# Kernel optimization log

Measured on AMD Instinct MI355X. Metric: run time of the kernel, lower is better.

Reference implementation:

```python
import jax, jax.numpy as jnp
import numpy as np

NUM_EMBEDDINGS = 8192
EMBEDDING_DIM = 512
COMMITMENT_COST = 0.25
BATCH = 32768


def setup_inputs() -> dict:
    key = jax.random.key(0)
    k_in, k_cb = jax.random.split(key)
    inputs = jax.random.normal(k_in, (BATCH, EMBEDDING_DIM), dtype=jnp.float32)
    # xavier_uniform_ on [num_embeddings, embedding_dim]
    limit = float(np.sqrt(6.0 / (NUM_EMBEDDINGS + EMBEDDING_DIM)))
    codebook = jax.random.uniform(k_cb, (NUM_EMBEDDINGS, EMBEDDING_DIM),
                                  dtype=jnp.float32, minval=-limit, maxval=limit)
    return {"inputs": inputs, "codebook": codebook}


def reference(inputs, codebook):
    # distances[b, n] = ||x_b||^2 + ||e_n||^2 - 2 x_b . e_n  (cdist^2 via matmul)
    distances = (jnp.sum(inputs ** 2, axis=1, keepdims=True)
                 + jnp.sum(codebook ** 2, axis=1)
                 - 2.0 * jnp.matmul(inputs, codebook.T))
    encoding_indices = jnp.argmin(distances, axis=1)  # [B]

    # one-hot @ codebook is just a row gather
    quantized = codebook[encoding_indices]  # [B, D]

    e_latent_loss = jnp.mean((jax.lax.stop_gradient(quantized) - inputs) ** 2)
    q_latent_loss = jnp.mean((quantized - jax.lax.stop_gradient(inputs)) ** 2)
    loss = q_latent_loss + COMMITMENT_COST * e_latent_loss

    # straight-through estimator
    quantized_st = inputs + jax.lax.stop_gradient(quantized - inputs)

    # avg_probs = mean over batch of one-hot encodings -> normalized bincount
    counts = jnp.zeros((NUM_EMBEDDINGS,), dtype=jnp.float32).at[encoding_indices].add(1.0)
    avg_probs = counts / BATCH
    perplexity = jnp.exp(-jnp.sum(avg_probs * jnp.log(avg_probs + 1e-10)))

    return quantized_st, loss, perplexity
```

## Files before the change

### kernel.cpp

```cpp
#include <hip/hip_runtime.h>
#include <math.h>

#define BATCH 32768
#define D 512
#define NE 8192
#define NSPLIT 4
#define ESPAN (NE / NSPLIT)
#define NT 64
#define KC 128
#define NPHASE ((ESPAN / NT) * 4)
#define MARGIN 1.6e-2f

typedef float    f32x4 __attribute__((ext_vector_type(4)));
typedef _Float16 f16x8 __attribute__((ext_vector_type(8)));

__device__ __forceinline__ void g2l16(const void* g, void* l) {
    __builtin_amdgcn_global_load_lds((const __attribute__((address_space(1))) void*)g,
                                     (__attribute__((address_space(3))) void*)l, 16, 0, 0);
}
__device__ __forceinline__ unsigned short f2h(float f) {
    union { _Float16 h; unsigned short u; } c; c.h = (_Float16)f; return c.u;
}

__global__ void vq_norms_kernel(const float* __restrict__ cb, float* __restrict__ norms) {
    int row  = blockIdx.x * 4 + (threadIdx.x >> 6);
    int lane = threadIdx.x & 63;
    const float4* p = (const float4*)(cb + (size_t)row * D);
    float s = 0.f;
#pragma unroll
    for (int i = 0; i < 2; ++i) {
        float4 v = p[lane + 64 * i];
        s += v.x * v.x + v.y * v.y + v.z * v.z + v.w * v.w;
    }
    for (int off = 32; off; off >>= 1) s += __shfl_down(s, off);
    if (lane == 0) norms[row] = s;
}

__global__ void vq_cvt_swz(const float* __restrict__ cb, unsigned short* __restrict__ eq) {
    int i = blockIdx.x * 256 + threadIdx.x;
    int n = i >> 6, g = i & 63;
    int ch = g >> 4;
    int sl = (g & 15) ^ (n & 15);
    const float4* sp = (const float4*)(cb + (size_t)n * D + g * 8);
    float4 a = sp[0], b = sp[1];
    ushort4* dp = (ushort4*)(eq + (size_t)n * D + ch * KC + sl * 8);
    dp[0] = make_ushort4(f2h(a.x), f2h(a.y), f2h(a.z), f2h(a.w));
    dp[1] = make_ushort4(f2h(b.x), f2h(b.y), f2h(b.z), f2h(b.w));
}

__global__ __launch_bounds__(256, 2)
void vq_topk2(const float* __restrict__ x, const unsigned short* __restrict__ eq,
              const float* __restrict__ norms, float4* __restrict__ cands) {
    __shared__ char arena[40960];
    unsigned short* es0 = (unsigned short*)arena;
    unsigned short* es1 = (unsigned short*)(arena + 16384);
    float*          nlds = (float*)(arena + 32768);

    const int t = threadIdx.x;
    const int w = t >> 6, lane = t & 63, l15 = lane & 15, l4 = lane >> 4;
    const int b = blockIdx.x;
    const int xcd = b & 7;
    const int sp  = xcd >> 1;
    const int rb  = ((b >> 3) << 1) | (xcd & 1);
    const size_t row0 = (size_t)rb * 128;
    const int nbase = sp * ESPAN;

#define STAGE(DST, STEP) do {                                                           \
        const int snt_ = (STEP) >> 2, sch_ = (STEP) & 3;                                \
        _Pragma("unroll")                                                               \
        for (int i_ = 0; i_ < 4; ++i_) {                                                \
            int c_ = i_ * 256 + t;                                                      \
            int row_ = c_ >> 4, sl_ = c_ & 15;                                          \
            g2l16(eq + (size_t)(nbase + snt_ * NT + row_) * D + sch_ * KC + sl_ * 8,    \
                  (DST) + (size_t)(i_ * 256 + w * 64) * 8);                             \
        }                                                                               \
    } while (0)

    STAGE(es0, 0);
#pragma unroll
    for (int i = 0; i < 2; ++i) {
        int c = i * 256 + t;
        g2l16(norms + nbase + c * 4, (char*)nlds + (size_t)(i * 256 + w * 64) * 16);
    }

    f16x8 af[2][16];
#pragma unroll
    for (int mi = 0; mi < 2; ++mi) {
        const float4* xp = (const float4*)(x + (row0 + w * 32 + mi * 16 + l15) * D);
#pragma unroll
        for (int ks = 0; ks < 16; ++ks) {
            float4 p0 = xp[ks * 8 + l4 * 2];
            float4 p1 = xp[ks * 8 + l4 * 2 + 1];
            f16x8 v;
            v[0] = (_Float16)p0.x; v[1] = (_Float16)p0.y;
            v[2] = (_Float16)p0.z; v[3] = (_Float16)p0.w;
            v[4] = (_Float16)p1.x; v[5] = (_Float16)p1.y;
            v[6] = (_Float16)p1.z; v[7] = (_Float16)p1.w;
            af[mi][ks] = v;
        }
    }

    float v1[8], v2[8];
    int   i1[8], i2[8];
#pragma unroll
    for (int s = 0; s < 8; ++s) { v1[s] = v2[s] = 3.4e38f; i1[s] = i2[s] = 0x7fffffff; }

    unsigned short* cur = es0;
    unsigned short* nxt = es1;

    for (int nt_ = 0; nt_ < ESPAN / NT; ++nt_) {
        f32x4 acc[2][4];
#pragma unroll
        for (int mi = 0; mi < 2; ++mi)
#pragma unroll
            for (int ni = 0; ni < 4; ++ni) acc[mi][ni] = (f32x4){0.f, 0.f, 0.f, 0.f};

#pragma unroll
        for (int ch = 0; ch < 4; ++ch) {
            const int step = nt_ * 4 + ch;
            asm volatile("s_waitcnt vmcnt(0)" ::: "memory");
            __builtin_amdgcn_s_barrier();
            __builtin_amdgcn_sched_barrier(0);
            if (step + 1 < NPHASE) STAGE(nxt, step + 1);
            __builtin_amdgcn_s_setprio(1);
#pragma unroll
            for (int ksb = 0; ksb < 4; ++ksb) {
                f16x8 bfr[4];
#pragma unroll
                for (int ni = 0; ni < 4; ++ni) {
                    int slot = ((ksb << 2) | l4) ^ l15;
                    bfr[ni] = *(const f16x8*)((const char*)cur + ni * 4096 + l15 * 256 + slot * 16);
                }
#pragma unroll
                for (int mi = 0; mi < 2; ++mi)
#pragma unroll
                    for (int ni = 0; ni < 4; ++ni)
                        acc[mi][ni] = __builtin_amdgcn_mfma_f32_16x16x32_f16(
                            af[mi][ch * 4 + ksb], bfr[ni], acc[mi][ni], 0, 0, 0);
            }
            __builtin_amdgcn_s_setprio(0);
            unsigned short* tswap = cur; cur = nxt; nxt = tswap;
        }

        const int n0 = nbase + nt_ * NT;
        float nn[4];
#pragma unroll
        for (int ni = 0; ni < 4; ++ni) nn[ni] = nlds[nt_ * 64 + ni * 16 + l15];
#pragma unroll
        for (int mi = 0; mi < 2; ++mi)
#pragma unroll
            for (int r = 0; r < 4; ++r) {
                int s = mi * 4 + r;
#pragma unroll
                for (int ni = 0; ni < 4; ++ni) {
                    float dd = fmaf(-2.f, acc[mi][ni][r], nn[ni]);
                    int   cc = n0 + ni * 16 + l15;
                    if (dd < v2[s]) {
                        bool b1 = dd < v1[s];
                        v2[s] = b1 ? v1[s] : dd; i2[s] = b1 ? i1[s] : cc;
                        v1[s] = b1 ? dd : v1[s]; i1[s] = b1 ? cc : i1[s];
                    }
                }
            }
    }
#undef STAGE

#pragma unroll
    for (int s = 0; s < 8; ++s) {
        int mi = s >> 2, r = s & 3;
        size_t rowc = row0 + w * 32 + mi * 16 + l4 * 4 + r;
        cands[rowc * 64 + sp * 16 + l15] =
            make_float4(v1[s], __int_as_float(i1[s]), v2[s], __int_as_float(i2[s]));
    }
}

__global__ __launch_bounds__(512)
void vq_finish(const float* __restrict__ x, const float* __restrict__ cb,
               const float* __restrict__ norms, const float4* __restrict__ cands,
               float* __restrict__ counts, float* __restrict__ psum, float* __restrict__ out) {
    __shared__ float red[8];
    const int t = threadIdx.x, w = t >> 6, lane = t & 63;
    const size_t row = (size_t)blockIdx.x * 8 + w;

    float4 c4 = cands[row * 64 + lane];
    float va = c4.x, vb = c4.z;
    int   ia = __float_as_int(c4.y), ib = __float_as_int(c4.w);
    float m = fminf(va, vb);
#pragma unroll
    for (int off = 1; off < 64; off <<= 1) m = fminf(m, __shfl_xor(m, off));
    const float thr = m + MARGIN;

    const float4* xp = (const float4*)(x + row * D);
    float4 xa = xp[lane * 2], xb = xp[lane * 2 + 1];

    float bd = 3.4e38f; int bi = 0x7fffffff;
#pragma unroll 1
    for (int q = 0; q < 2; ++q) {
        unsigned long long mk = __ballot((q == 0 ? va : vb) <= thr);
        while (mk) {
            int src = __builtin_ctzll(mk);
            mk &= mk - 1;
            int ci = __shfl(q == 0 ? ia : ib, src);
            const float4* ep = (const float4*)(cb + (size_t)ci * D);
            float4 ea = ep[lane * 2], eb = ep[lane * 2 + 1];
            float s = 0.f;
            s = fmaf(xa.x, ea.x, s); s = fmaf(xa.y, ea.y, s);
            s = fmaf(xa.z, ea.z, s); s = fmaf(xa.w, ea.w, s);
            s = fmaf(xb.x, eb.x, s); s = fmaf(xb.y, eb.y, s);
            s = fmaf(xb.z, eb.z, s); s = fmaf(xb.w, eb.w, s);
#pragma unroll
            for (int off = 1; off < 64; off <<= 1) s += __shfl_xor(s, off);
            float dd = fmaf(-2.f, s, norms[ci]);
            if (dd < bd || (dd == bd && ci < bi)) { bd = dd; bi = ci; }
        }
    }

    const float4* qp = (const float4*)(cb + (size_t)bi * D);
    float4 qa = qp[lane * 2], qb = qp[lane * 2 + 1];
    float4* op = (float4*)(out + row * D);
    float s2 = 0.f;
    float4 oa, ob;
    {
        float d0 = qa.x - xa.x; oa.x = xa.x + d0; s2 = fmaf(d0, d0, s2);
        float d1 = qa.y - xa.y; oa.y = xa.y + d1; s2 = fmaf(d1, d1, s2);
        float d2 = qa.z - xa.z; oa.z = xa.z + d2; s2 = fmaf(d2, d2, s2);
        float d3 = qa.w - xa.w; oa.w = xa.w + d3; s2 = fmaf(d3, d3, s2);
        float d4 = qb.x - xb.x; ob.x = xb.x + d4; s2 = fmaf(d4, d4, s2);
        float d5 = qb.y - xb.y; ob.y = xb.y + d5; s2 = fmaf(d5, d5, s2);
        float d6 = qb.z - xb.z; ob.z = xb.z + d6; s2 = fmaf(d6, d6, s2);
        float d7 = qb.w - xb.w; ob.w = xb.w + d7; s2 = fmaf(d7, d7, s2);
    }
    op[lane * 2] = oa; op[lane * 2 + 1] = ob;
    for (int off = 32; off; off >>= 1) s2 += __shfl_down(s2, off);
    if (lane == 0) {
        red[w] = s2;
        atomicAdd(&counts[bi], 1.0f);
    }
    __syncthreads();
    if (t == 0) {
        float s = 0.f;
#pragma unroll
        for (int i = 0; i < 8; ++i) s += red[i];
        psum[blockIdx.x] = s;
    }
}

__global__ void vq_finalize_kernel(const float* __restrict__ counts, const float* __restrict__ psum,
                                   float* __restrict__ out2) {
    __shared__ float rede[256];
    __shared__ float reds[256];
    float se = 0.f, ss = 0.f;
    for (int i = threadIdx.x; i < NE; i += 256) {
        float p = counts[i] * (1.0f / (float)BATCH);
        se += p * logf(p + 1e-10f);
    }
    for (int i = threadIdx.x; i < 4096; i += 256) ss += psum[i];
    rede[threadIdx.x] = se; reds[threadIdx.x] = ss;
    __syncthreads();
    for (int off = 128; off; off >>= 1) {
        if (threadIdx.x < off) {
            rede[threadIdx.x] += rede[threadIdx.x + off];
            reds[threadIdx.x] += reds[threadIdx.x + off];
        }
        __syncthreads();
    }
    if (threadIdx.x == 0) {
        out2[0] = 1.25f * reds[0] * (1.0f / (float)((size_t)BATCH * D));
        out2[1] = expf(-rede[0]);
    }
}

#define BM 64
#define BN 64
#define BK 16
#define LDSP 68
__global__ __launch_bounds__(256)
void vq_argmin_kernel(const float* __restrict__ x, const float* __restrict__ cb,
                      const float* __restrict__ norms, int* __restrict__ out_idx) {
    __shared__ float xs[BK * LDSP];
    __shared__ float es[BK * LDSP];
    __shared__ float rv[BM][16];
    __shared__ int   ri[BM][16];
    const int t = threadIdx.x, tx = t & 15, ty = t >> 4;
    const int row0 = blockIdx.x * BM, ldrow = t >> 2, ldq = t & 3;
    float minv[4]; int mini[4];
#pragma unroll
    for (int i = 0; i < 4; ++i) { minv[i] = 3.4e38f; mini[i] = 0; }
    for (int n0 = 0; n0 < NE; n0 += BN) {
        float acc[4][4];
#pragma unroll
        for (int i = 0; i < 4; ++i)
#pragma unroll
            for (int j = 0; j < 4; ++j) acc[i][j] = 0.f;
        for (int kk = 0; kk < D; kk += BK) {
            __syncthreads();
            float4 xv = *(const float4*)&x [(size_t)(row0 + ldrow) * D + kk + ldq * 4];
            float4 ev = *(const float4*)&cb[(size_t)(n0   + ldrow) * D + kk + ldq * 4];
            const float* xvp = (const float*)&xv;
            const float* evp = (const float*)&ev;
#pragma unroll
            for (int j = 0; j < 4; ++j) {
                xs[(ldq * 4 + j) * LDSP + ldrow] = xvp[j];
                es[(ldq * 4 + j) * LDSP + ldrow] = evp[j];
            }
            __syncthreads();
#pragma unroll
            for (int k = 0; k < BK; ++k) {
                float4 xr4 = *(const float4*)&xs[k * LDSP + ty * 4];
                float4 er4 = *(const float4*)&es[k * LDSP + tx * 4];
                const float xr[4] = {xr4.x, xr4.y, xr4.z, xr4.w};
                const float er[4] = {er4.x, er4.y, er4.z, er4.w};
#pragma unroll
                for (int i = 0; i < 4; ++i)
#pragma unroll
                    for (int j = 0; j < 4; ++j)
                        acc[i][j] = fmaf(xr[i], er[j], acc[i][j]);
            }
        }
#pragma unroll
        for (int j = 0; j < 4; ++j) {
            int n = n0 + tx * 4 + j;
            float nnv = norms[n];
#pragma unroll
            for (int i = 0; i < 4; ++i) {
                float dd = fmaf(-2.f, acc[i][j], nnv);
                if (dd < minv[i]) { minv[i] = dd; mini[i] = n; }
            }
        }
    }
    __syncthreads();
#pragma unroll
    for (int i = 0; i < 4; ++i) { rv[ty * 4 + i][tx] = minv[i]; ri[ty * 4 + i][tx] = mini[i]; }
    __syncthreads();
    if (t < BM) {
        float bv = rv[t][0]; int bi = ri[t][0];
#pragma unroll
        for (int j = 1; j < 16; ++j) {
            float v = rv[t][j]; int iz = ri[t][j];
            if (v < bv || (v == bv && iz < bi)) { bv = v; bi = iz; }
        }
        out_idx[row0 + t] = bi;
    }
}

__global__ void vq_gather_kernel(const float* __restrict__ x, const float* __restrict__ cb,
                                 const int* __restrict__ idx, float* __restrict__ out,
                                 float* __restrict__ counts, float* __restrict__ psum) {
    const int b = blockIdx.x, lane = threadIdx.x;
    const int e = idx[b];
    const float4* xp = (const float4*)(x  + (size_t)b * D);
    const float4* qp = (const float4*)(cb + (size_t)e * D);
    float4*       op = (float4*)(out + (size_t)b * D);
    float s = 0.f;
#pragma unroll
    for (int i = 0; i < 2; ++i) {
        float4 xv = xp[lane + 64 * i];
        float4 qv = qp[lane + 64 * i];
        float4 ov;
        float dx = qv.x - xv.x; ov.x = xv.x + dx; s = fmaf(dx, dx, s);
        float dy = qv.y - xv.y; ov.y = xv.y + dy; s = fmaf(dy, dy, s);
        float dz = qv.z - xv.z; ov.z = xv.z + dz; s = fmaf(dz, dz, s);
        float dw = qv.w - xv.w; ov.w = xv.w + dw; s = fmaf(dw, dw, s);
        op[lane + 64 * i] = ov;
    }
    for (int off = 32; off; off >>= 1) s += __shfl_down(s, off);
    if (lane == 0) {
        atomicAdd(&psum[0], s);
        atomicAdd(&counts[e], 1.0f);
    }
}

extern "C" void kernel_launch(void* const* d_in, const int* in_sizes, int n_in,
                              void* d_out, int out_size, void* d_ws, size_t ws_size,
                              hipStream_t stream) {
    const float* x  = (const float*)d_in[0];
    const float* cb = (const float*)d_in[1];
    float* out = (float*)d_out;

    char* ws = (char*)d_ws;
    float*  norms  = (float*)ws;
    float*  counts = (float*)(ws + 32768);
    float*  psum   = (float*)(ws + 65536);
    int*    idx    = (int*)(ws + 81920);
    float4* cands  = (float4*)(ws + 262144);
    unsigned short* eq = (unsigned short*)(ws + 33816576);
    const size_t WS_NEED = 42205184;

    hipMemsetAsync(counts, 0, NE * sizeof(float), stream);
    vq_norms_kernel<<<NE / 4, 256, 0, stream>>>(cb, norms);

    if (ws_size >= WS_NEED) {
        vq_cvt_swz<<<NE * 64 / 256, 256, 0, stream>>>(cb, eq);
        vq_topk2<<<1024, 256, 0, stream>>>(x, eq, norms, cands);
        vq_finish<<<BATCH / 8, 512, 0, stream>>>(x, cb, norms, cands, counts, psum, out);
    } else {
        hipMemsetAsync(psum, 0, 4096 * sizeof(float), stream);
        vq_argmin_kernel<<<BATCH / BM, 256, 0, stream>>>(x, cb, norms, idx);
        vq_gather_kernel<<<BATCH, 64, 0, stream>>>(x, cb, idx, out, counts, psum);
    }
    vq_finalize_kernel<<<1, 256, 0, stream>>>(counts, psum, out + (size_t)BATCH * D);
}
```

Measured before the change: 424.8 us.

## Fuse codebook prep kernels, fold norms into accumulator init, prefetch LDS fragments

Merges the codebook norm and fp16 swizzle-convert kernels into one prep kernel so the codebook is read once and one launch is saved. In the top-k kernel, the -0.5*norm bias is preloaded into the MFMA accumulators and the running top-2 becomes a max search, removing the per-element fma and the LDS norm staging. Norms for the next tile are prefetched from global memory in registers. B fragments are double-buffered across k-substeps so LDS reads overlap the MFMAs. This raises register pressure, and candidate values are rescaled by -2 at the end, which changes rounding slightly relative to the finish kernel's margin.

```diff
diff --git a/kernel.cpp b/kernel.cpp
--- a/kernel.cpp
+++ b/kernel.cpp
@@ -22,39 +22,31 @@
     union { _Float16 h; unsigned short u; } c; c.h = (_Float16)f; return c.u;
 }
 
-__global__ void vq_norms_kernel(const float* __restrict__ cb, float* __restrict__ norms) {
-    int row  = blockIdx.x * 4 + (threadIdx.x >> 6);
-    int lane = threadIdx.x & 63;
-    const float4* p = (const float4*)(cb + (size_t)row * D);
-    float s = 0.f;
-#pragma unroll
-    for (int i = 0; i < 2; ++i) {
-        float4 v = p[lane + 64 * i];
-        s += v.x * v.x + v.y * v.y + v.z * v.z + v.w * v.w;
-    }
+__global__ void vq_prep(const float* __restrict__ cb, unsigned short* __restrict__ eq,
+                        float* __restrict__ norms) {
+    const int row = blockIdx.x * 4 + (threadIdx.x >> 6);
+    const int g   = threadIdx.x & 63;
+    const float4* sp = (const float4*)(cb + (size_t)row * D + g * 8);
+    float4 a = sp[0], b = sp[1];
+    float s = a.x * a.x + a.y * a.y + a.z * a.z + a.w * a.w
+            + b.x * b.x + b.y * b.y + b.z * b.z + b.w * b.w;
     for (int off = 32; off; off >>= 1) s += __shfl_down(s, off);
-    if (lane == 0) norms[row] = s;
-}
-
-__global__ void vq_cvt_swz(const float* __restrict__ cb, unsigned short* __restrict__ eq) {
-    int i = blockIdx.x * 256 + threadIdx.x;
-    int n = i >> 6, g = i & 63;
-    int ch = g >> 4;
-    int sl = (g & 15) ^ (n & 15);
-    const float4* sp = (const float4*)(cb + (size_t)n * D + g * 8);
-    float4 a = sp[0], b = sp[1];
-    ushort4* dp = (ushort4*)(eq + (size_t)n * D + ch * KC + sl * 8);
+    if (g == 0) norms[row] = s;
+    const int ch = g >> 4;
+    const int sl = (g & 15) ^ (row & 15);
+    ushort4* dp = (ushort4*)(eq + (size_t)row * D + ch * KC + sl * 8);
     dp[0] = make_ushort4(f2h(a.x), f2h(a.y), f2h(a.z), f2h(a.w));
     dp[1] = make_ushort4(f2h(b.x), f2h(b.y), f2h(b.z), f2h(b.w));
 }
+
+struct Frag4 { f16x8 v[4]; };
 
 __global__ __launch_bounds__(256, 2)
 void vq_topk2(const float* __restrict__ x, const unsigned short* __restrict__ eq,
               const float* __restrict__ norms, float4* __restrict__ cands) {
-    __shared__ char arena[40960];
+    __shared__ char arena[32768];
     unsigned short* es0 = (unsigned short*)arena;
     unsigned short* es1 = (unsigned short*)(arena + 16384);
-    float*          nlds = (float*)(arena + 32768);
 
     const int t = threadIdx.x;
     const int w = t >> 6, lane = t & 63, l15 = lane & 15, l4 = lane >> 4;
@@ -77,11 +69,6 @@
     } while (0)
 
     STAGE(es0, 0);
-#pragma unroll
-    for (int i = 0; i < 2; ++i) {
-        int c = i * 256 + t;
-        g2l16(norms + nbase + c * 4, (char*)nlds + (size_t)(i * 256 + w * 64) * 16);
-    }
 
     f16x8 af[2][16];
 #pragma unroll
@@ -100,10 +87,14 @@
         }
     }
 
+    float nnc[4];
+#pragma unroll
+    for (int ni = 0; ni < 4; ++ni) nnc[ni] = -0.5f * norms[nbase + ni * 16 + l15];
+
     float v1[8], v2[8];
     int   i1[8], i2[8];
 #pragma unroll
-    for (int s = 0; s < 8; ++s) { v1[s] = v2[s] = 3.4e38f; i1[s] = i2[s] = 0x7fffffff; }
+    for (int s = 0; s < 8; ++s) { v1[s] = v2[s] = -3.4e38f; i1[s] = i2[s] = 0x7fffffff; }
 
     unsigned short* cur = es0;
     unsigned short* nxt = es1;
@@ -113,7 +104,11 @@
 #pragma unroll
         for (int mi = 0; mi < 2; ++mi)
 #pragma unroll
-            for (int ni = 0; ni < 4; ++ni) acc[mi][ni] = (f32x4){0.f, 0.f, 0.f, 0.f};
+            for (int ni = 0; ni < 4; ++ni) {
+                float h = nnc[ni];
+                acc[mi][ni] = (f32x4){h, h, h, h};
+            }
+        float nnn[4];
 
 #pragma unroll
         for (int ch = 0; ch < 4; ++ch) {
@@ -122,30 +117,41 @@
             __builtin_amdgcn_s_barrier();
             __builtin_amdgcn_sched_barrier(0);
             if (step + 1 < NPHASE) STAGE(nxt, step + 1);
+            if (ch == 0 && nt_ + 1 < ESPAN / NT) {
+#pragma unroll
+                for (int ni = 0; ni < 4; ++ni)
+                    nnn[ni] = -0.5f * norms[nbase + (nt_ + 1) * NT + ni * 16 + l15];
+            }
             __builtin_amdgcn_s_setprio(1);
+            const char* esp = (const char*)cur;
+            Frag4 fa, fb;
+#pragma unroll
+            for (int ni = 0; ni < 4; ++ni) {
+                int slot = l4 ^ l15;
+                fa.v[ni] = *(const f16x8*)(esp + ni * 4096 + l15 * 256 + slot * 16);
+            }
 #pragma unroll
             for (int ksb = 0; ksb < 4; ++ksb) {
-                f16x8 bfr[4];
-#pragma unroll
-                for (int ni = 0; ni < 4; ++ni) {
-                    int slot = ((ksb << 2) | l4) ^ l15;
-                    bfr[ni] = *(const f16x8*)((const char*)cur + ni * 4096 + l15 * 256 + slot * 16);
+                if (ksb < 3) {
+#pragma unroll
+                    for (int ni = 0; ni < 4; ++ni) {
+                        int slot = (((ksb + 1) << 2) | l4) ^ l15;
+                        fb.v[ni] = *(const f16x8*)(esp + ni * 4096 + l15 * 256 + slot * 16);
+                    }
                 }
 #pragma unroll
                 for (int mi = 0; mi < 2; ++mi)
 #pragma unroll
                     for (int ni = 0; ni < 4; ++ni)
                         acc[mi][ni] = __builtin_amdgcn_mfma_f32_16x16x32_f16(
-                            af[mi][ch * 4 + ksb], bfr[ni], acc[mi][ni], 0, 0, 0);
+                            af[mi][ch * 4 + ksb], fa.v[ni], acc[mi][ni], 0, 0, 0);
+                if (ksb < 3) fa = fb;
             }
             __builtin_amdgcn_s_setprio(0);
             unsigned short* tswap = cur; cur = nxt; nxt = tswap;
         }
 
         const int n0 = nbase + nt_ * NT;
-        float nn[4];
-#pragma unroll
-        for (int ni = 0; ni < 4; ++ni) nn[ni] = nlds[nt_ * 64 + ni * 16 + l15];
 #pragma unroll
         for (int mi = 0; mi < 2; ++mi)
 #pragma unroll
@@ -153,15 +159,17 @@
                 int s = mi * 4 + r;
 #pragma unroll
                 for (int ni = 0; ni < 4; ++ni) {
-                    float dd = fmaf(-2.f, acc[mi][ni][r], nn[ni]);
-                    int   cc = n0 + ni * 16 + l15;
-                    if (dd < v2[s]) {
-                        bool b1 = dd < v1[s];
-                        v2[s] = b1 ? v1[s] : dd; i2[s] = b1 ? i1[s] : cc;
-                        v1[s] = b1 ? dd : v1[s]; i1[s] = b1 ? cc : i1[s];
+                    float a = acc[mi][ni][r];
+                    int  cc = n0 + ni * 16 + l15;
+                    if (a > v2[s]) {
+                        bool b1 = a > v1[s];
+                        v2[s] = b1 ? v1[s] : a; i2[s] = b1 ? i1[s] : cc;
+                        v1[s] = b1 ? a : v1[s]; i1[s] = b1 ? cc : i1[s];
                     }
                 }
             }
+#pragma unroll
+        for (int ni = 0; ni < 4; ++ni) nnc[ni] = nnn[ni];
     }
 #undef STAGE
 
@@ -170,7 +178,7 @@
         int mi = s >> 2, r = s & 3;
         size_t rowc = row0 + w * 32 + mi * 16 + l4 * 4 + r;
         cands[rowc * 64 + sp * 16 + l15] =
-            make_float4(v1[s], __int_as_float(i1[s]), v2[s], __int_as_float(i2[s]));
+            make_float4(-2.f * v1[s], __int_as_float(i1[s]), -2.f * v2[s], __int_as_float(i2[s]));
     }
 }
 
@@ -270,6 +278,20 @@
     }
 }
 
+__global__ void vq_norms_kernel(const float* __restrict__ cb, float* __restrict__ norms) {
+    int row  = blockIdx.x * 4 + (threadIdx.x >> 6);
+    int lane = threadIdx.x & 63;
+    const float4* p = (const float4*)(cb + (size_t)row * D);
+    float s = 0.f;
+#pragma unroll
+    for (int i = 0; i < 2; ++i) {
+        float4 v = p[lane + 64 * i];
+        s += v.x * v.x + v.y * v.y + v.z * v.z + v.w * v.w;
+    }
+    for (int off = 32; off; off >>= 1) s += __shfl_down(s, off);
+    if (lane == 0) norms[row] = s;
+}
+
 #define BM 64
 #define BN 64
 #define BK 16
@@ -387,14 +409,14 @@
     const size_t WS_NEED = 42205184;
 
     hipMemsetAsync(counts, 0, NE * sizeof(float), stream);
-    vq_norms_kernel<<<NE / 4, 256, 0, stream>>>(cb, norms);
 
     if (ws_size >= WS_NEED) {
-        vq_cvt_swz<<<NE * 64 / 256, 256, 0, stream>>>(cb, eq);
+        vq_prep<<<NE / 4, 256, 0, stream>>>(cb, eq, norms);
         vq_topk2<<<1024, 256, 0, stream>>>(x, eq, norms, cands);
         vq_finish<<<BATCH / 8, 512, 0, stream>>>(x, cb, norms, cands, counts, psum, out);
     } else {
         hipMemsetAsync(psum, 0, 4096 * sizeof(float), stream);
+        vq_norms_kernel<<<NE / 4, 256, 0, stream>>>(cb, norms);
         vq_argmin_kernel<<<BATCH / BM, 256, 0, stream>>>(x, cb, norms, idx);
         vq_gather_kernel<<<BATCH, 64, 0, stream>>>(x, cb, idx, out, counts, psum);
     }
```

Measured after the change: 438.5 us. 3.2% more time.
